# Performance work log

Hardware: AMD Instinct MI355X
Metric: run time of the kernel (lower is better)

Reference implementation:

```python
import jax, jax.numpy as jnp
import numpy as np

B, NCAP, LV, LT, C = 64, 64, 197, 32, 512
NSP = LV - 1          # 196 spatial patches
NUM_KEEP = 98         # ceil(196 * sparse_ratio=0.5)
KEEPED = 49           # int(196 * aggr_ratio=0.5 * sparse_ratio=0.5)
HID = 102             # int(512 * dim_ratio=0.2)
LN_EPS = 1e-5


def _normalize(x):
    # torch F.normalize: x / max(||x||, 1e-12)
    return x / jnp.maximum(jnp.linalg.norm(x, axis=-1, keepdims=True), 1e-12)


def setup_inputs() -> dict:
    key = jax.random.key(0)
    ks = jax.random.split(key, 8)
    def rn(k, shape, s=0.02):
        return jax.random.normal(k, shape, jnp.float32) * s
    return {
        "img_embs": jax.random.normal(ks[0], (B, LV, C), jnp.float32),
        "cap_embs": jax.random.normal(ks[1], (NCAP, LT, C), jnp.float32),
        "cap_lens": jnp.full((NCAP,), LT, jnp.int32),
        "ln_gamma": jnp.ones((C,), jnp.float32),
        "ln_beta": jnp.zeros((C,), jnp.float32),
        "w1": rn(ks[2], (C, HID)), "b1": jnp.zeros((HID,), jnp.float32),
        "w2": rn(ks[3], (HID, KEEPED)), "b2": jnp.zeros((KEEPED,), jnp.float32),
        "aggr_scale": jnp.ones((1, 1, 1), jnp.float32),
        "wi2t": rn(ks[4], (C, C)), "bi2t": jnp.zeros((C,), jnp.float32),
        "wt2i": rn(ks[5], (C, C)), "bt2i": jnp.zeros((C,), jnp.float32),
        "temp": jnp.ones((1, 1, 1), jnp.float32),
    }


def _forward(img_embs, cap_embs, ln_gamma, ln_beta, w1, b1, w2, b2,
             aggr_scale, wi2t, bi2t, wt2i, bt2i, temp):
    img_norm = _normalize(img_embs)
    img_cls = img_embs[:, 0:1]              # [B,1,C]  has_cls_token branch
    img_sp = img_embs[:, 1:]                # [B,196,C]
    img_sp_norm = img_norm[:, 1:]
    # use_cls_as_glob_embd: global = normalized CLS (no grad)
    glo = jax.lax.stop_gradient(img_norm[:, 0:1])
    attn_x = jax.lax.stop_gradient(jnp.sum(glo * img_sp_norm, -1))  # [B,196]
    cap_norm = _normalize(cap_embs)
    bidx = jnp.arange(B)[:, None]

    def ln(x):
        m = x.mean(-1, keepdims=True)
        v = jnp.var(x, axis=-1, keepdims=True)
        return (x - m) / jnp.sqrt(v + LN_EPS) * ln_gamma + ln_beta

    def per_caption(cap_i, cap_i_norm):
        # cap_i, cap_i_norm: [LT, C]
        cap_glo = jax.lax.stop_gradient(_normalize(cap_i[0:1]))           # [1,C]
        attn_y = jax.lax.stop_gradient(jnp.sum(cap_glo[None] * img_sp_norm, -1))  # [B,196]
        # --- TokenSparse ---
        score = attn_x + attn_y
        order = jnp.argsort(-score, axis=1)                              # descending
        keep, nonkeep = order[:, :NUM_KEEP], order[:, NUM_KEEP:]
        sel = img_sp[bidx, keep]                                          # [B,98,C]
        non = img_sp[bidx, nonkeep]                                       # [B,98,C]
        non_score = jnp.take_along_axis(score, nonkeep, 1)
        extra = jnp.sum(non * jax.nn.softmax(non_score, axis=1)[..., None],
                        axis=1, keepdims=True)                            # [B,1,C]
        # --- TokenAggregation ---
        h = jax.nn.gelu(ln(sel) @ w1 + b1, approximate=False)             # [B,98,HID]
        w = jnp.swapaxes(h @ w2 + b2, 1, 2) * aggr_scale                  # [B,49,98]
        aggr = jax.nn.softmax(w, axis=2) @ sel                            # [B,49,C]
        # [cls, aggr, extra] -> [B,51,C], then normalize
        sel_tok = _normalize(jnp.concatenate([img_cls, aggr, extra], 1))
        Ls = sel_tok.shape[1]
        # --- 'attn' similarity ---
        cap_exp = jnp.broadcast_to(cap_i_norm[None], (B, LT, C))
        st = jnp.swapaxes(sel_tok, 1, 2)                                  # [B,C,51]
        c2i = jax.nn.leaky_relu(cap_exp @ st, negative_slope=0.1)         # [B,LT,51]
        a_i2t = jax.nn.softmax((cap_exp @ wi2t + bi2t) @ st / temp, axis=1)
        a_t2i = jax.nn.softmax((cap_exp @ wt2i + bt2i) @ st / temp, axis=2)
        return jnp.sum(a_i2t * c2i / Ls + a_t2i * c2i / LT, axis=(1, 2))  # [B]

    sims = jax.vmap(per_caption)(cap_embs, cap_norm)                      # [NCAP,B]
    return sims.T                                                         # [B,NCAP]


def reference(img_embs, cap_embs, cap_lens, ln_gamma, ln_beta, w1, b1, w2, b2,
              aggr_scale, wi2t, bi2t, wt2i, bt2i, temp):
    # cap_lens are all LT (static shapes); eval-mode output: similarity matrix.
    return _forward(img_embs, cap_embs, ln_gamma, ln_beta, w1, b1, w2, b2,
                    aggr_scale, wi2t, bi2t, wt2i, bt2i, temp)
```

## Files before the change

### kernel.cpp

```cpp
#include <hip/hip_runtime.h>
#include <math.h>

#define B     64
#define NCAP  64
#define LV    197
#define LT    32
#define C     512
#define NSP   196
#define NKEEP 98
#define HID   102
#define KEEPED 49

#define OFF_ATTNX   12608
#define OFF_WSMAT   25152
#define OFF_WT      639808
#define OFF_GLOT    1688384
#define OFF_ATTNYT  1721152
#define OFF_IMGT    14164800
#define OFF_QBB     17834816
#define OFF_QCAP    19407680
#define OFF_W1TF    19931968
#define OFF_W2TF    19960640

typedef unsigned int u32;
typedef unsigned short u16;
typedef __bf16 bf16x8 __attribute__((ext_vector_type(8)));
typedef float f32x4 __attribute__((ext_vector_type(4)));
typedef unsigned int uint4v __attribute__((ext_vector_type(4)));

__device__ __forceinline__ u16 f2bf(float f) {
    u32 u = __builtin_bit_cast(u32, f);
    return (u16)((u + 0x7FFFu + ((u >> 16) & 1u)) >> 16);
}
__device__ __forceinline__ bf16x8 ld_bf8(const u16* p) {
    uint4v v = *reinterpret_cast<const uint4v*>(p);
    return __builtin_bit_cast(bf16x8, v);
}

__device__ __forceinline__ float gelu_exact(float x) {
    return 0.5f * x * (1.f + erff(x * 0.70710678118654752f));
}

__global__ __launch_bounds__(256) void k_pre(const float* __restrict__ cap,
                                             const float* __restrict__ wi2t,
                                             const float* __restrict__ wt2i,
                                             const float* __restrict__ w1,
                                             const float* __restrict__ w2,
                                             float* __restrict__ gloT,
                                             u16* __restrict__ Qbbf,
                                             u16* __restrict__ Qcap,
                                             u16* __restrict__ wT,
                                             u16* __restrict__ w1Tf,
                                             u16* __restrict__ w2Tf) {
    int idx = blockIdx.x, t = threadIdx.x;
    __shared__ __align__(16) u16 shb[64 * 65];

    if (idx < 512) {
        int e = idx, i = e >> 3, tg = e & 7;
        int lane = t & 63, wv = t >> 6;
        int tt = tg * 4 + wv;
        const float* row = cap + ((size_t)i * LT + tt) * C;
        float v[8]; float ss = 0.f;
#pragma unroll
        for (int q = 0; q < 8; ++q) { v[q] = row[lane + 64 * q]; ss += v[q] * v[q]; }
        for (int o = 32; o > 0; o >>= 1) ss += __shfl_down(ss, o);
        ss = __shfl(ss, 0);
        float inv = 1.f / fmaxf(sqrtf(ss), 1e-12f);
        u16* qrow = Qcap + ((size_t)i * 32 + tt) * C;
        int mi = tt >> 4, l15f = tt & 15;
        u16* qfb = Qbbf + (size_t)(i * 6 + mi) * 16 * 512;
#pragma unroll
        for (int q = 0; q < 8; ++q) {
            float n = v[q] * inv;
            u16 nb = f2bf(n);
            int c = lane + 64 * q;
            qrow[c] = nb;
            int ks = c >> 5, quadf = (c >> 3) & 3, jf = c & 7;
            qfb[(size_t)ks * 512 + (quadf * 16 + l15f) * 8 + jf] = nb;
            if (tt == 0) gloT[(c >> 2) * (NCAP * 4) + i * 4 + (c & 3)] = n;
        }
    } else if (idx < 640) {
        int e = idx - 512;
        int mat = e >> 6, ty = e & 63, jg = ty >> 3, cg = ty & 7;
        const float* W = mat ? wt2i : wi2t;
        u16 (*tile)[65] = (u16(*)[65])shb;
        for (int f = t; f < 4096; f += 256) {
            int cc2 = f >> 6, jj = f & 63;
            tile[jj][cc2] = f2bf(W[(size_t)(cg * 64 + cc2) * 512 + jg * 64 + jj]);
        }
        __syncthreads();
        for (int f = t; f < 4096; f += 256) {
            int jj = f >> 6, cc2 = f & 63;
            wT[((size_t)mat * 512 + jg * 64 + jj) * 512 + cg * 64 + cc2] = tile[jj][cc2];
        }
    } else if (idx < 647) {
        int nt = idx - 640;
        u32* outp = (u32*)w1Tf + (size_t)nt * 16 * 256;
        for (int f = t; f < 16 * 256; f += 256) {
            int ks = f >> 8, g = f & 255;
            int lane_o = g >> 2, j2 = g & 3;
            int l15o = lane_o & 15, quado = lane_o >> 4;
            int kk = ks * 32 + quado * 8 + 2 * j2;
            int n = nt * 16 + l15o;
            u32 lo = 0, hi = 0;
            if (n < HID) {
                lo = f2bf(w1[(size_t)kk * HID + n]);
                hi = f2bf(w1[(size_t)(kk + 1) * HID + n]);
            }
            outp[ks * 256 + g] = lo | (hi << 16);
        }
    } else {
        u32* outp = (u32*)w2Tf;
        for (int f = t; f < 16 * 256; f += 256) {
            int tile = f >> 8, g = f & 255;
            int nt2 = tile >> 2, ks2 = tile & 3;
            int lane_o = g >> 2, j2 = g & 3;
            int l15o = lane_o & 15, quado = lane_o >> 4;
            int kk0 = ks2 * 32 + quado * 8 + 2 * j2;
            int n = nt2 * 16 + l15o;
            u32 lo = 0, hi = 0;
            if (n < KEEPED) {
                if (kk0 < HID)     lo = f2bf(w2[(size_t)kk0 * KEEPED + n]);
                if (kk0 + 1 < HID) hi = f2bf(w2[(size_t)(kk0 + 1) * KEEPED + n]);
            }
            outp[tile * 256 + g] = lo | (hi << 16);
        }
    }
}

__global__ __launch_bounds__(512) void k_mid(const float* __restrict__ img,
                                             const u16* __restrict__ wT,
                                             const float* __restrict__ bi2t,
                                             const float* __restrict__ bt2i,
                                             const u16* __restrict__ Qcap,
                                             u16* __restrict__ Qbbf,
                                             const u16* __restrict__ w1Tf,
                                             const u16* __restrict__ w2Tf,
                                             const float* __restrict__ gamw,
                                             const float* __restrict__ betw,
                                             const float* __restrict__ b1,
                                             const float* __restrict__ b2,
                                             const float* __restrict__ scale_p,
                                             const float* __restrict__ gloT,
                                             float* __restrict__ attn_x,
                                             u16* __restrict__ WsM16,
                                             float* __restrict__ attn_yT,
                                             u16* __restrict__ imgTf) {
    int idx = blockIdx.x, t = threadIdx.x;
    __shared__ __align__(16) u16 shu[64 * 224];

    if (idx < 256) {
        int i = idx & 63, p = idx >> 6;
        int lane = t & 63, wu = t >> 6;
        int l15 = lane & 15, quad = lane >> 4;
        int mat = wu >> 2;
        int miq = (wu >> 1) & 1;
        int nh  = wu & 1;
        int ni0 = p * 8 + nh * 4;
        const u16* Arow = Qcap + ((size_t)i * 32 + miq * 16 + l15) * 512;
        const u16* Wm   = wT + (size_t)mat * 512 * 512;
        f32x4 acc[4];
#pragma unroll
        for (int n = 0; n < 4; ++n) acc[n] = (f32x4){0.f, 0.f, 0.f, 0.f};
        bf16x8 A = ld_bf8(Arow + quad * 8);
        bf16x8 Bf[4];
#pragma unroll
        for (int n = 0; n < 4; ++n)
            Bf[n] = ld_bf8(Wm + (size_t)((ni0 + n) * 16 + l15) * 512 + quad * 8);
        for (int ks = 0; ks < 16; ++ks) {
            bf16x8 An; bf16x8 Bn[4];
            if (ks < 15) {
                An = ld_bf8(Arow + (ks + 1) * 32 + quad * 8);
#pragma unroll
                for (int n = 0; n < 4; ++n)
                    Bn[n] = ld_bf8(Wm + (size_t)((ni0 + n) * 16 + l15) * 512 + (ks + 1) * 32 + quad * 8);
            }
#pragma unroll
            for (int n = 0; n < 4; ++n)
                acc[n] = __builtin_amdgcn_mfma_f32_16x16x32_bf16(A, Bf[n], acc[n], 0, 0, 0);
            A = An;
#pragma unroll
            for (int n = 0; n < 4; ++n) Bf[n] = Bn[n];
        }
        const float* bias = mat ? bt2i : bi2t;
#pragma unroll
        for (int n = 0; n < 4; ++n) {
            int j = (ni0 + n) * 16 + l15;
            float bj = bias[j];
            int ksf = j >> 5, quadf = (j >> 3) & 3, jf = j & 7;
#pragma unroll
            for (int r = 0; r < 4; ++r) {
                int q = 32 + mat * 32 + miq * 16 + quad * 4 + r;
                int mi = q >> 4, l15f = q & 15;
                Qbbf[(size_t)((i * 6 + mi) * 16 + ksf) * 512 + (quadf * 16 + l15f) * 8 + jf]
                    = f2bf(acc[n][r] + bj);
            }
        }
    } else if (idx < 1088) {
        int e = idx - 256;
        int b = e / 13, sg = e - b * 13;
        int s0 = sg * 16;
        u16* LNb = shu;
        u16* Hb  = shu + 16 * 520;
        int lane = t & 63, wu = t >> 6;
        int l15 = lane & 15, quad = lane >> 4;

        {
            int rr0 = 2 * wu, rr1 = 2 * wu + 1;
            int sA = s0 + rr0, sB = s0 + rr1;
            int sAc = sA < NSP ? sA : NSP - 1;
            int sBc = sB < NSP ? sB : NSP - 1;
            const float* rowA = img + ((size_t)b * LV + 1 + sAc) * C;
            const float* rowB = img + ((size_t)b * LV + 1 + sBc) * C;
            const float* cls  = img + (size_t)b * LV * C;
            float v0[8], v1[8];
            float sm0 = 0, ss0 = 0, dd0 = 0, sm1 = 0, ss1 = 0, dd1 = 0, sc = 0;
#pragma unroll
            for (int q = 0; q < 8; ++q) {
                int c = lane + 64 * q;
                float cv = cls[c];
                v0[q] = rowA[c]; v1[q] = rowB[c];
                sm0 += v0[q]; ss0 += v0[q] * v0[q]; dd0 += v0[q] * cv;
                sm1 += v1[q]; ss1 += v1[q] * v1[q]; dd1 += v1[q] * cv;
                sc  += cv * cv;
            }
            for (int o = 32; o > 0; o >>= 1) {
                sm0 += __shfl_down(sm0, o); ss0 += __shfl_down(ss0, o); dd0 += __shfl_down(dd0, o);
                sm1 += __shfl_down(sm1, o); ss1 += __shfl_down(ss1, o); dd1 += __shfl_down(dd1, o);
                sc  += __shfl_down(sc, o);
            }
            sm0 = __shfl(sm0, 0); ss0 = __shfl(ss0, 0);
            sm1 = __shfl(sm1, 0); ss1 = __shfl(ss1, 0);
            float mean0 = sm0 * (1.f / C);
            float rstd0 = 1.f / sqrtf(ss0 * (1.f / C) - mean0 * mean0 + 1e-5f);
            float mean1 = sm1 * (1.f / C);
            float rstd1 = 1.f / sqrtf(ss1 * (1.f / C) - mean1 * mean1 + 1e-5f);
            if (lane == 0) {
                float inv0 = 1.f / fmaxf(sqrtf(sc), 1e-12f);
                if (sA < NSP) attn_x[b * NSP + sA] = dd0 * inv0 * (1.f / fmaxf(sqrtf(ss0), 1e-12f));
                if (sB < NSP) attn_x[b * NSP + sB] = dd1 * inv0 * (1.f / fmaxf(sqrtf(ss1), 1e-12f));
            }
#pragma unroll
            for (int q = 0; q < 8; ++q) {
                int c = lane + 64 * q;
                float g = gamw[c], be = betw[c];
                LNb[rr0 * 520 + c] = f2bf((v0[q] - mean0) * rstd0 * g + be);
                LNb[rr1 * 520 + c] = f2bf((v1[q] - mean1) * rstd1 * g + be);
            }
        }
        __syncthreads();
        if (wu < 7) {
            const u16* W1b = w1Tf + (size_t)wu * 16 * 512;
            f32x4 h4 = (f32x4){0.f, 0.f, 0.f, 0.f};
            for (int ks = 0; ks < 16; ++ks) {
                bf16x8 A = ld_bf8(LNb + l15 * 520 + ks * 32 + quad * 8);
                bf16x8 Bv = ld_bf8(W1b + ks * 512 + lane * 8);
                h4 = __builtin_amdgcn_mfma_f32_16x16x32_bf16(A, Bv, h4, 0, 0, 0);
            }
            int col = wu * 16 + l15;
            if (col < HID) {
                float bb = b1[col];
#pragma unroll
                for (int r = 0; r < 4; ++r)
                    Hb[(quad * 4 + r) * 136 + col] = f2bf(gelu_exact(h4[r] + bb));
            } else {
#pragma unroll
                for (int r = 0; r < 4; ++r) Hb[(quad * 4 + r) * 136 + col] = 0;
            }
        } else {
            for (int f = lane; f < 16 * 24; f += 64) {
                int row = f / 24, cc = 112 + f % 24;
                Hb[row * 136 + cc] = 0;
            }
        }
        __syncthreads();
        if (wu < 4) {
            const u16* W2b = w2Tf + (size_t)wu * 4 * 512;
            f32x4 a2 = (f32x4){0.f, 0.f, 0.f, 0.f};
            for (int ks2 = 0; ks2 < 4; ++ks2) {
                bf16x8 A2 = ld_bf8(Hb + l15 * 136 + ks2 * 32 + quad * 8);
                bf16x8 B2 = ld_bf8(W2b + ks2 * 512 + lane * 8);
                a2 = __builtin_amdgcn_mfma_f32_16x16x32_bf16(A2, B2, a2, 0, 0, 0);
            }
            int k = wu * 16 + l15;
            if (k < KEEPED) {
                float scale = scale_p[0], bk = b2[k];
#pragma unroll
                for (int r = 0; r < 4; ++r) {
                    int row = quad * 4 + r;
                    if (s0 + row < NSP)
                        WsM16[((size_t)b * NSP + s0 + row) * 49 + k] = f2bf(expf((a2[r] + bk) * scale));
                }
            }
        }
    } else if (idx < 2688) {
        int e = idx - 1088;
        int b = e / 25;
        int s0 = (e - b * 25) * 8;
        int R = NSP - s0; if (R > 8) R = 8;
        float (*xr)[C] = (float(*)[C])shu;
        float* rnorm = (float*)shu + 4096;

        for (int f = t; f < R * C; f += 512) {
            int rr = f >> 9, c = f & 511;
            xr[rr][c] = img[((size_t)b * LV + 1 + s0 + rr) * C + c];
        }
        __syncthreads();
        {
            int row = t >> 6, l = t & 63;
            if (row < R) {
                float ss = 0.f;
                for (int c = l; c < C; c += 64) { float v = xr[row][c]; ss += v * v; }
                for (int o = 32; o > 0; o >>= 1) ss += __shfl_down(ss, o);
                if (l == 0) rnorm[row] = 1.f / fmaxf(sqrtf(ss), 1e-12f);
            }
        }
        __syncthreads();
        for (int f = t; f < R * C; f += 512) {
            int rr = f >> 9, c = f & 511;
            xr[rr][c] *= rnorm[rr];
        }
        __syncthreads();
        int i = t & 63, w = t >> 6;
        if (w < R) {
            float a0 = 0.f;
            const float4* g4 = (const float4*)gloT;
            const float4* x4 = (const float4*)xr[w];
            for (int c4 = 0; c4 < C / 4; ++c4) {
                float4 g = g4[c4 * NCAP + i];
                float4 x0 = x4[c4];
                a0 += x0.x * g.x + x0.y * g.y + x0.z * g.z + x0.w * g.w;
            }
            attn_yT[((size_t)b * NCAP + i) * NSP + s0 + w] = a0;
        }
    } else {
        int e = idx - 2688;
        int b = e >> 3, cg = e & 7;
        for (int f = t; f < 64 * 27; f += 512) shu[(f / 27) * 224 + 197 + (f % 27)] = 0;
        int cc = t & 63;
        for (int sb = t >> 6; sb < 197; sb += 8) {
            float v = img[((size_t)b * LV + sb) * C + cg * 64 + cc];
            shu[cc * 224 + sb] = f2bf(v);
        }
        __syncthreads();
        const u32* Tu = (const u32*)shu;
        u32* outp = (u32*)imgTf + (size_t)b * 7 * 32 * 256;
        for (int f = t; f < 7 * 4 * 256; f += 512) {
            int ks = f >> 10, rem = f & 1023;
            int ctl = rem >> 8, g = rem & 255;
            int lane_o = g >> 2, j2 = g & 3;
            int quad_o = lane_o >> 4, l15_o = lane_o & 15;
            int ccl = ctl * 16 + l15_o;
            int s = ks * 32 + quad_o * 8 + 2 * j2;
            u32 v = Tu[ccl * 112 + (s >> 1)];
            outp[(size_t)(ks * 32 + cg * 4 + ctl) * 256 + g] = v;
        }
    }
}

__global__ __launch_bounds__(512, 4) void k_main(const float* __restrict__ attn_x,
                                                 const float* __restrict__ attn_yT,
                                                 const u16* __restrict__ WsM16,
                                                 const u16* __restrict__ imgTf,
                                                 const u16* __restrict__ Qbbf,
                                                 const float* __restrict__ temp_p,
                                                 float* __restrict__ out) {
    int lin = blockIdx.x + NCAP * blockIdx.y;
    int b = (lin & 7) * 8 + ((lin >> 3) & 7);
    int i = lin >> 6;
    int t = threadIdx.x;
    int lane = t & 63, wu = t >> 6;
    int l15 = lane & 15, quad = lane >> 4;

    __shared__ __align__(16) u16 TnBuf[51 * 520];
    __shared__ float invn[64];
    __shared__ float redw[8];

    u16*   Pf   = TnBuf;
    float* ULDS = (float*)TnBuf;
    float* scoreS = (float*)(TnBuf + 24000);
    short* rnkH   = (short*)(TnBuf + 24392);
    u16*   keepL  = (u16*)  (TnBuf + 24784);
    u16*   nonL   = (u16*)  (TnBuf + 24882);
    float* snon   = (float*)(TnBuf + 25000);
    float* rowsq  = (float*)(TnBuf + 25372);

    const u16* imgTb = imgTf + (size_t)b * 7 * 32 * 512;
    bf16x8 Bc[4], Bn[4];
#pragma unroll
    for (int nj = 0; nj < 4; ++nj)
        Bc[nj] = ld_bf8(imgTb + (size_t)(wu * 4 + nj) * 512 + lane * 8);

    {
        uint4v* Pfv = (uint4v*)Pf;
        for (int f = t; f < 51 * 232 / 8; f += 512) Pfv[f] = (uint4v){0, 0, 0, 0};
    }
    if (t < NSP)
        scoreS[t] = attn_x[b * NSP + t] + attn_yT[((size_t)b * NCAP + i) * NSP + t];
    __syncthreads();
    if (t < 2 * NSP) {
        int half = (t >= NSP) ? 1 : 0;
        int s = t - half * NSP;
        float sv = scoreS[s];
        const float2* sc2 = (const float2*)scoreS;
        int base = half ? 49 : 0;
        int r = 0;
        for (int u2 = base; u2 < base + 49; ++u2) {
            float2 o = sc2[u2];
            int u = 2 * u2;
            r += (o.x > sv) || (o.x == sv && u < s);
            r += (o.y > sv) || (o.y == sv && (u + 1) < s);
        }
        rnkH[half * NSP + s] = (short)r;
    }
    __syncthreads();
    if (t < NSP) {
        int r = rnkH[t] + rnkH[NSP + t];
        if (r < NKEEP) keepL[r] = (u16)t;
        else { nonL[r - NKEEP] = (u16)t; snon[r - NKEEP] = scoreS[t]; }
    }
    __syncthreads();
    if (t == 0) Pf[0] = 0x3F80;
    if (t < NKEEP) Pf[50 * 232 + 1 + nonL[t]] = f2bf(expf(snon[t]));
    {
        int j = t / KEEPED, k = t - (t / KEEPED) * KEEPED;
#pragma unroll
        for (int it = 0; it < 10; ++it) {
            if (j < NKEEP) {
                int s = keepL[j];
                Pf[(1 + k) * 232 + 1 + s] = WsM16[((size_t)b * NSP + s) * 49 + k];
            }
            j += 10; k += 22;
            if (k >= KEEPED) { k -= KEEPED; ++j; }
        }
    }
    __syncthreads();

    f32x4 acc[4][4];
#pragma unroll
    for (int mi = 0; mi < 4; ++mi)
#pragma unroll
        for (int nj = 0; nj < 4; ++nj) acc[mi][nj] = (f32x4){0.f, 0.f, 0.f, 0.f};

    for (int ks = 0; ks < 7; ++ks) {
        if (ks < 6) {
#pragma unroll
            for (int nj = 0; nj < 4; ++nj)
                Bn[nj] = ld_bf8(imgTb + (size_t)((ks + 1) * 32 + wu * 4 + nj) * 512 + lane * 8);
        }
        bf16x8 Afr[4];
#pragma unroll
        for (int mi = 0; mi < 4; ++mi)
            Afr[mi] = ld_bf8(Pf + (mi * 16 + l15) * 232 + ks * 32 + quad * 8);
#pragma unroll
        for (int nj = 0; nj < 4; ++nj)
#pragma unroll
            for (int mi = 0; mi < 4; ++mi)
                acc[mi][nj] = __builtin_amdgcn_mfma_f32_16x16x32_bf16(Afr[mi], Bc[nj], acc[mi][nj], 0, 0, 0);
#pragma unroll
        for (int nj = 0; nj < 4; ++nj) Bc[nj] = Bn[nj];
    }

#pragma unroll
    for (int mi = 0; mi < 4; ++mi)
#pragma unroll
        for (int r = 0; r < 4; ++r) {
            float s = acc[mi][0][r] * acc[mi][0][r] + acc[mi][1][r] * acc[mi][1][r]
                    + acc[mi][2][r] * acc[mi][2][r] + acc[mi][3][r] * acc[mi][3][r];
            s += __shfl_down(s, 8); s += __shfl_down(s, 4);
            s += __shfl_down(s, 2); s += __shfl_down(s, 1);
            if (l15 == 0) rowsq[wu * 64 + mi * 16 + quad * 4 + r] = s;
        }
    __syncthreads();
    if (t < 64) {
        float s = 0.f;
#pragma unroll
        for (int w2 = 0; w2 < 8; ++w2) s += rowsq[w2 * 64 + t];
        invn[t] = 1.f / fmaxf(sqrtf(s), 1e-12f);
    }
    __syncthreads();

#pragma unroll
    for (int mi = 0; mi < 4; ++mi)
#pragma unroll
        for (int r = 0; r < 4; ++r) {
            int row = mi * 16 + quad * 4 + r;
            if (row < 51) {
                float iv = invn[row];
#pragma unroll
                for (int nj = 0; nj < 4; ++nj)
                    TnBuf[row * 520 + (wu * 4 + nj) * 16 + l15] = f2bf(acc[mi][nj][r] * iv);
            }
        }
    __syncthreads();

    const u16* Qbf = Qbbf + (size_t)i * 6 * 16 * 512;
    f32x4 ua[3];
#pragma unroll
    for (int e = 0; e < 3; ++e) ua[e] = (f32x4){0.f, 0.f, 0.f, 0.f};

    if (wu < 6) {
        const u16* Ar = Qbf + (size_t)wu * 16 * 512 + lane * 8;
        bf16x8 Aa = ld_bf8(Ar + 0 * 512);
        bf16x8 Ab = ld_bf8(Ar + 1 * 512);
        bf16x8 Ac = ld_bf8(Ar + 2 * 512);
        bf16x8 Ad = ld_bf8(Ar + 3 * 512);
#pragma unroll
        for (int g = 0; g < 4; ++g) {
            bf16x8 Na, Nb, Nc, Nd;
            if (g < 3) {
                Na = ld_bf8(Ar + (g * 4 + 4) * 512);
                Nb = ld_bf8(Ar + (g * 4 + 5) * 512);
                Nc = ld_bf8(Ar + (g * 4 + 6) * 512);
                Nd = ld_bf8(Ar + (g * 4 + 7) * 512);
            }
#pragma unroll
            for (int e = 0; e < 3; ++e) {
                const u16* Tb = TnBuf + (e * 16 + l15) * 520 + quad * 8;
                ua[e] = __builtin_amdgcn_mfma_f32_16x16x32_bf16(Aa, ld_bf8(Tb + (g * 4 + 0) * 32), ua[e], 0, 0, 0);
                ua[e] = __builtin_amdgcn_mfma_f32_16x16x32_bf16(Ab, ld_bf8(Tb + (g * 4 + 1) * 32), ua[e], 0, 0, 0);
                ua[e] = __builtin_amdgcn_mfma_f32_16x16x32_bf16(Ac, ld_bf8(Tb + (g * 4 + 2) * 32), ua[e], 0, 0, 0);
                ua[e] = __builtin_amdgcn_mfma_f32_16x16x32_bf16(Ad, ld_bf8(Tb + (g * 4 + 3) * 32), ua[e], 0, 0, 0);
            }
            Aa = Na; Ab = Nb; Ac = Nc; Ad = Nd;
        }
    } else {
        int w2 = wu - 6;
        int rowB = 48 + l15; if (rowB > 50) rowB = 50;
        const u16* Ar0 = Qbf + (size_t)(3 * w2 + 0) * 16 * 512 + lane * 8;
        const u16* Ar1 = Qbf + (size_t)(3 * w2 + 1) * 16 * 512 + lane * 8;
        const u16* Ar2 = Qbf + (size_t)(3 * w2 + 2) * 16 * 512 + lane * 8;
        bf16x8 Af0 = ld_bf8(Ar0);
        bf16x8 Af1 = ld_bf8(Ar1);
        bf16x8 Af2 = ld_bf8(Ar2);
        for (int ks = 0; ks < 16; ++ks) {
            bf16x8 An0, An1, An2;
            if (ks < 15) {
                An0 = ld_bf8(Ar0 + (ks + 1) * 512);
                An1 = ld_bf8(Ar1 + (ks + 1) * 512);
                An2 = ld_bf8(Ar2 + (ks + 1) * 512);
            }
            bf16x8 Bf = ld_bf8(TnBuf + rowB * 520 + ks * 32 + quad * 8);
            ua[0] = __builtin_amdgcn_mfma_f32_16x16x32_bf16(Af0, Bf, ua[0], 0, 0, 0);
            ua[1] = __builtin_amdgcn_mfma_f32_16x16x32_bf16(Af1, Bf, ua[1], 0, 0, 0);
            ua[2] = __builtin_amdgcn_mfma_f32_16x16x32_bf16(Af2, Bf, ua[2], 0, 0, 0);
            Af0 = An0; Af1 = An1; Af2 = An2;
        }
    }
    __syncthreads();

    if (wu < 6) {
#pragma unroll
        for (int e = 0; e < 3; ++e) {
            int l = e * 16 + l15;
            int q0 = wu * 16 + quad * 4;
#pragma unroll
            for (int r = 0; r < 4; ++r) ULDS[(q0 + r) * 52 + l] = ua[e][r];
        }
    } else {
        int l = 48 + l15;
        if (l < 51) {
            int w2 = wu - 6;
#pragma unroll
            for (int e = 0; e < 3; ++e) {
                int q0 = (3 * w2 + e) * 16 + quad * 4;
#pragma unroll
                for (int r = 0; r < 4; ++r) ULDS[(q0 + r) * 52 + l] = ua[e][r];
            }
        }
    }
    __syncthreads();

    float invT = 1.f / temp_p[0];
    if (t < 408) {
        int l = t >> 3, sub = t & 7;
        float vbuf[4]; float mm = -1e30f;
#pragma unroll
        for (int q = 0; q < 4; ++q) {
            float v = ULDS[(32 + sub + 8 * q) * 52 + l] * invT;
            vbuf[q] = v;
            mm = fmaxf(mm, v);
        }
#pragma unroll
        for (int o = 1; o < 8; o <<= 1) mm = fmaxf(mm, __shfl_xor(mm, o, 8));
        float e[4]; float z = 0.f;
#pragma unroll
        for (int q = 0; q < 4; ++q) { e[q] = expf(vbuf[q] - mm); z += e[q]; }
#pragma unroll
        for (int o = 1; o < 8; o <<= 1) z += __shfl_xor(z, o, 8);
        float iz = 1.f / z;
#pragma unroll
        for (int q = 0; q < 4; ++q) ULDS[(32 + sub + 8 * q) * 52 + l] = e[q] * iz;
    }
    if (t < 256) {
        int u = t >> 3, sub = t & 7;
        float vbuf[7]; int cnt = 0; float mm = -1e30f;
        for (int l = sub; l < 51; l += 8) {
            float v = ULDS[(64 + u) * 52 + l] * invT;
            vbuf[cnt++] = v;
            mm = fmaxf(mm, v);
        }
#pragma unroll
        for (int o = 1; o < 8; o <<= 1) mm = fmaxf(mm, __shfl_xor(mm, o, 8));
        float e[7]; float z = 0.f;
        for (int q = 0; q < cnt; ++q) { e[q] = expf(vbuf[q] - mm); z += e[q]; }
#pragma unroll
        for (int o = 1; o < 8; o <<= 1) z += __shfl_xor(z, o, 8);
        float iz = 1.f / z;
        { int q = 0;
          for (int l = sub; l < 51; l += 8) { ULDS[(64 + u) * 52 + l] = e[q] * iz; ++q; } }
    }
    __syncthreads();

    float part = 0.f;
    {
        int u = t / 51, l = t - (t / 51) * 51;
        while (u < LT) {
            float u0 = ULDS[u * 52 + l];
            float c2 = (u0 > 0.f) ? u0 : 0.1f * u0;
            float av = ULDS[(32 + u) * 52 + l];
            float bv = ULDS[(64 + u) * 52 + l];
            part += c2 * (av * (1.f / 51.f) + bv * (1.f / 32.f));
            u += 10; l += 2;
            if (l >= 51) { l -= 51; ++u; }
        }
    }
    for (int o = 32; o > 0; o >>= 1) part += __shfl_down(part, o);
    if (lane == 0) redw[wu] = part;
    __syncthreads();
    if (t == 0) {
        float s = 0.f;
#pragma unroll
        for (int w2 = 0; w2 < 8; ++w2) s += redw[w2];
        out[b * NCAP + i] = s;
    }
}

extern "C" void kernel_launch(void* const* d_in, const int* in_sizes, int n_in,
                              void* d_out, int out_size, void* d_ws, size_t ws_size,
                              hipStream_t stream) {
    const float* img        = (const float*)d_in[0];
    const float* cap        = (const float*)d_in[1];
    const float* gamw       = (const float*)d_in[3];
    const float* betw       = (const float*)d_in[4];
    const float* w1         = (const float*)d_in[5];
    const float* b1         = (const float*)d_in[6];
    const float* w2         = (const float*)d_in[7];
    const float* b2         = (const float*)d_in[8];
    const float* aggr_scale = (const float*)d_in[9];
    const float* wi2t       = (const float*)d_in[10];
    const float* bi2t       = (const float*)d_in[11];
    const float* wt2i       = (const float*)d_in[12];
    const float* bt2i       = (const float*)d_in[13];
    const float* temp       = (const float*)d_in[14];
    float* out = (float*)d_out;

    float* ws      = (float*)d_ws;
    float* attn_x  = ws + OFF_ATTNX;
    u16*   WsM16   = (u16*)(ws + OFF_WSMAT);
    u16*   wT      = (u16*)(ws + OFF_WT);
    float* gloT    = ws + OFF_GLOT;
    float* attn_yT = ws + OFF_ATTNYT;
    u16*   imgTf   = (u16*)(ws + OFF_IMGT);
    u16*   Qbbf    = (u16*)(ws + OFF_QBB);
    u16*   Qcap    = (u16*)(ws + OFF_QCAP);
    u16*   w1Tf    = (u16*)(ws + OFF_W1TF);
    u16*   w2Tf    = (u16*)(ws + OFF_W2TF);

    k_pre<<<dim3(648), dim3(256), 0, stream>>>(cap, wi2t, wt2i, w1, w2,
                                               gloT, Qbbf, Qcap, wT, w1Tf, w2Tf);
    k_mid<<<dim3(3200), dim3(512), 0, stream>>>(img, wT, bi2t, bt2i, Qcap, Qbbf,
                                                w1Tf, w2Tf, gamw, betw, b1, b2, aggr_scale,
                                                gloT, attn_x, WsM16, attn_yT, imgTf);
    k_main<<<dim3(NCAP, B), dim3(512), 0, stream>>>(attn_x, attn_yT, WsM16, imgTf, Qbbf, temp, out);
}
```

Baseline: 344.0 us.

## Split token GEMM into two row halves to cut registers and raise occupancy

Launch bounds move from 4 to 6 blocks per SM. To fit that register budget, the 64-row token aggregation GEMM is split into two passes of 32 rows each (upper rows first, then lower), halving the accumulator array, and the row-norm scratch is reused in LDS. Register prefetch double-buffering is dropped in both GEMM phases. The imgT B-fragments are now loaded from global twice, and the lost software pipelining may expose latency, in exchange for more resident waves.

```diff
diff --git a/kernel.cpp b/kernel.cpp
--- a/kernel.cpp
+++ b/kernel.cpp
@@ -358,7 +358,7 @@
     }
 }
 
-__global__ __launch_bounds__(512, 4) void k_main(const float* __restrict__ attn_x,
+__global__ __launch_bounds__(512, 6) void k_main(const float* __restrict__ attn_x,
                                                  const float* __restrict__ attn_yT,
                                                  const u16* __restrict__ WsM16,
                                                  const u16* __restrict__ imgTf,
@@ -383,13 +383,10 @@
     u16*   keepL  = (u16*)  (TnBuf + 24784);
     u16*   nonL   = (u16*)  (TnBuf + 24882);
     float* snon   = (float*)(TnBuf + 25000);
-    float* rowsq  = (float*)(TnBuf + 25372);
+    float* rowsqA = (float*)(TnBuf + 25372);
+    float* rowsqB = (float*)TnBuf;
 
     const u16* imgTb = imgTf + (size_t)b * 7 * 32 * 512;
-    bf16x8 Bc[4], Bn[4];
-#pragma unroll
-    for (int nj = 0; nj < 4; ++nj)
-        Bc[nj] = ld_bf8(imgTb + (size_t)(wu * 4 + nj) * 512 + lane * 8);
 
     {
         uint4v* Pfv = (uint4v*)Pf;
@@ -436,61 +433,102 @@
     }
     __syncthreads();
 
-    f32x4 acc[4][4];
-#pragma unroll
-    for (int mi = 0; mi < 4; ++mi)
-#pragma unroll
-        for (int nj = 0; nj < 4; ++nj) acc[mi][nj] = (f32x4){0.f, 0.f, 0.f, 0.f};
+    f32x4 acc2[2][4];
+#pragma unroll
+    for (int m = 0; m < 2; ++m)
+#pragma unroll
+        for (int nj = 0; nj < 4; ++nj) acc2[m][nj] = (f32x4){0.f, 0.f, 0.f, 0.f};
 
     for (int ks = 0; ks < 7; ++ks) {
-        if (ks < 6) {
-#pragma unroll
-            for (int nj = 0; nj < 4; ++nj)
-                Bn[nj] = ld_bf8(imgTb + (size_t)((ks + 1) * 32 + wu * 4 + nj) * 512 + lane * 8);
-        }
-        bf16x8 Afr[4];
-#pragma unroll
-        for (int mi = 0; mi < 4; ++mi)
-            Afr[mi] = ld_bf8(Pf + (mi * 16 + l15) * 232 + ks * 32 + quad * 8);
+        bf16x8 Bc[4];
 #pragma unroll
         for (int nj = 0; nj < 4; ++nj)
-#pragma unroll
-            for (int mi = 0; mi < 4; ++mi)
-                acc[mi][nj] = __builtin_amdgcn_mfma_f32_16x16x32_bf16(Afr[mi], Bc[nj], acc[mi][nj], 0, 0, 0);
-#pragma unroll
-        for (int nj = 0; nj < 4; ++nj) Bc[nj] = Bn[nj];
-    }
-
-#pragma unroll
-    for (int mi = 0; mi < 4; ++mi)
+            Bc[nj] = ld_bf8(imgTb + (size_t)(ks * 32 + wu * 4 + nj) * 512 + lane * 8);
+        bf16x8 Af0 = ld_bf8(Pf + (32 + l15) * 232 + ks * 32 + quad * 8);
+        bf16x8 Af1 = ld_bf8(Pf + (48 + l15) * 232 + ks * 32 + quad * 8);
+#pragma unroll
+        for (int nj = 0; nj < 4; ++nj) {
+            acc2[0][nj] = __builtin_amdgcn_mfma_f32_16x16x32_bf16(Af0, Bc[nj], acc2[0][nj], 0, 0, 0);
+            acc2[1][nj] = __builtin_amdgcn_mfma_f32_16x16x32_bf16(Af1, Bc[nj], acc2[1][nj], 0, 0, 0);
+        }
+    }
+#pragma unroll
+    for (int m = 0; m < 2; ++m)
 #pragma unroll
         for (int r = 0; r < 4; ++r) {
-            float s = acc[mi][0][r] * acc[mi][0][r] + acc[mi][1][r] * acc[mi][1][r]
-                    + acc[mi][2][r] * acc[mi][2][r] + acc[mi][3][r] * acc[mi][3][r];
+            float s = acc2[m][0][r] * acc2[m][0][r] + acc2[m][1][r] * acc2[m][1][r]
+                    + acc2[m][2][r] * acc2[m][2][r] + acc2[m][3][r] * acc2[m][3][r];
             s += __shfl_down(s, 8); s += __shfl_down(s, 4);
             s += __shfl_down(s, 2); s += __shfl_down(s, 1);
-            if (l15 == 0) rowsq[wu * 64 + mi * 16 + quad * 4 + r] = s;
-        }
-    __syncthreads();
-    if (t < 64) {
+            if (l15 == 0) rowsqA[wu * 32 + m * 16 + quad * 4 + r] = s;
+        }
+    __syncthreads();
+    if (t < 32) {
         float s = 0.f;
 #pragma unroll
-        for (int w2 = 0; w2 < 8; ++w2) s += rowsq[w2 * 64 + t];
-        invn[t] = 1.f / fmaxf(sqrtf(s), 1e-12f);
-    }
-    __syncthreads();
-
-#pragma unroll
-    for (int mi = 0; mi < 4; ++mi)
+        for (int w2 = 0; w2 < 8; ++w2) s += rowsqA[w2 * 32 + t];
+        invn[32 + t] = 1.f / fmaxf(sqrtf(s), 1e-12f);
+    }
+    __syncthreads();
+#pragma unroll
+    for (int m = 0; m < 2; ++m)
 #pragma unroll
         for (int r = 0; r < 4; ++r) {
-            int row = mi * 16 + quad * 4 + r;
+            int row = 32 + m * 16 + quad * 4 + r;
             if (row < 51) {
                 float iv = invn[row];
 #pragma unroll
                 for (int nj = 0; nj < 4; ++nj)
-                    TnBuf[row * 520 + (wu * 4 + nj) * 16 + l15] = f2bf(acc[mi][nj][r] * iv);
-            }
+                    TnBuf[row * 520 + (wu * 4 + nj) * 16 + l15] = f2bf(acc2[m][nj][r] * iv);
+            }
+        }
+
+#pragma unroll
+    for (int m = 0; m < 2; ++m)
+#pragma unroll
+        for (int nj = 0; nj < 4; ++nj) acc2[m][nj] = (f32x4){0.f, 0.f, 0.f, 0.f};
+
+    for (int ks = 0; ks < 7; ++ks) {
+        bf16x8 Bc[4];
+#pragma unroll
+        for (int nj = 0; nj < 4; ++nj)
+            Bc[nj] = ld_bf8(imgTb + (size_t)(ks * 32 + wu * 4 + nj) * 512 + lane * 8);
+        bf16x8 Af0 = ld_bf8(Pf + (0 + l15) * 232 + ks * 32 + quad * 8);
+        bf16x8 Af1 = ld_bf8(Pf + (16 + l15) * 232 + ks * 32 + quad * 8);
+#pragma unroll
+        for (int nj = 0; nj < 4; ++nj) {
+            acc2[0][nj] = __builtin_amdgcn_mfma_f32_16x16x32_bf16(Af0, Bc[nj], acc2[0][nj], 0, 0, 0);
+            acc2[1][nj] = __builtin_amdgcn_mfma_f32_16x16x32_bf16(Af1, Bc[nj], acc2[1][nj], 0, 0, 0);
+        }
+    }
+    __syncthreads();
+#pragma unroll
+    for (int m = 0; m < 2; ++m)
+#pragma unroll
+        for (int r = 0; r < 4; ++r) {
+            float s = acc2[m][0][r] * acc2[m][0][r] + acc2[m][1][r] * acc2[m][1][r]
+                    + acc2[m][2][r] * acc2[m][2][r] + acc2[m][3][r] * acc2[m][3][r];
+            s += __shfl_down(s, 8); s += __shfl_down(s, 4);
+            s += __shfl_down(s, 2); s += __shfl_down(s, 1);
+            if (l15 == 0) rowsqB[wu * 32 + m * 16 + quad * 4 + r] = s;
+        }
+    __syncthreads();
+    if (t < 32) {
+        float s = 0.f;
+#pragma unroll
+        for (int w2 = 0; w2 < 8; ++w2) s += rowsqB[w2 * 32 + t];
+        invn[t] = 1.f / fmaxf(sqrtf(s), 1e-12f);
+    }
+    __syncthreads();
+#pragma unroll
+    for (int m = 0; m < 2; ++m)
+#pragma unroll
+        for (int r = 0; r < 4; ++r) {
+            int row = m * 16 + quad * 4 + r;
+            float iv = invn[row];
+#pragma unroll
+            for (int nj = 0; nj < 4; ++nj)
+                TnBuf[row * 520 + (wu * 4 + nj) * 16 + l15] = f2bf(acc2[m][nj][r] * iv);
         }
     __syncthreads();
 
@@ -501,28 +539,16 @@
 
     if (wu < 6) {
         const u16* Ar = Qbf + (size_t)wu * 16 * 512 + lane * 8;
-        bf16x8 Aa = ld_bf8(Ar + 0 * 512);
-        bf16x8 Ab = ld_bf8(Ar + 1 * 512);
-        bf16x8 Ac = ld_bf8(Ar + 2 * 512);
-        bf16x8 Ad = ld_bf8(Ar + 3 * 512);
-#pragma unroll
-        for (int g = 0; g < 4; ++g) {
-            bf16x8 Na, Nb, Nc, Nd;
-            if (g < 3) {
-                Na = ld_bf8(Ar + (g * 4 + 4) * 512);
-                Nb = ld_bf8(Ar + (g * 4 + 5) * 512);
-                Nc = ld_bf8(Ar + (g * 4 + 6) * 512);
-                Nd = ld_bf8(Ar + (g * 4 + 7) * 512);
-            }
+        bf16x8 Af = ld_bf8(Ar);
+        for (int ks = 0; ks < 16; ++ks) {
+            bf16x8 An;
+            if (ks < 15) An = ld_bf8(Ar + (ks + 1) * 512);
 #pragma unroll
             for (int e = 0; e < 3; ++e) {
-                const u16* Tb = TnBuf + (e * 16 + l15) * 520 + quad * 8;
-                ua[e] = __builtin_amdgcn_mfma_f32_16x16x32_bf16(Aa, ld_bf8(Tb + (g * 4 + 0) * 32), ua[e], 0, 0, 0);
-                ua[e] = __builtin_amdgcn_mfma_f32_16x16x32_bf16(Ab, ld_bf8(Tb + (g * 4 + 1) * 32), ua[e], 0, 0, 0);
-                ua[e] = __builtin_amdgcn_mfma_f32_16x16x32_bf16(Ac, ld_bf8(Tb + (g * 4 + 2) * 32), ua[e], 0, 0, 0);
-                ua[e] = __builtin_amdgcn_mfma_f32_16x16x32_bf16(Ad, ld_bf8(Tb + (g * 4 + 3) * 32), ua[e], 0, 0, 0);
-            }
-            Aa = Na; Ab = Nb; Ac = Nc; Ad = Nd;
+                bf16x8 Bf = ld_bf8(TnBuf + (e * 16 + l15) * 520 + ks * 32 + quad * 8);
+                ua[e] = __builtin_amdgcn_mfma_f32_16x16x32_bf16(Af, Bf, ua[e], 0, 0, 0);
+            }
+            Af = An;
         }
     } else {
         int w2 = wu - 6;
@@ -530,21 +556,11 @@
         const u16* Ar0 = Qbf + (size_t)(3 * w2 + 0) * 16 * 512 + lane * 8;
         const u16* Ar1 = Qbf + (size_t)(3 * w2 + 1) * 16 * 512 + lane * 8;
         const u16* Ar2 = Qbf + (size_t)(3 * w2 + 2) * 16 * 512 + lane * 8;
-        bf16x8 Af0 = ld_bf8(Ar0);
-        bf16x8 Af1 = ld_bf8(Ar1);
-        bf16x8 Af2 = ld_bf8(Ar2);
         for (int ks = 0; ks < 16; ++ks) {
-            bf16x8 An0, An1, An2;
-            if (ks < 15) {
-                An0 = ld_bf8(Ar0 + (ks + 1) * 512);
-                An1 = ld_bf8(Ar1 + (ks + 1) * 512);
-                An2 = ld_bf8(Ar2 + (ks + 1) * 512);
-            }
             bf16x8 Bf = ld_bf8(TnBuf + rowB * 520 + ks * 32 + quad * 8);
-            ua[0] = __builtin_amdgcn_mfma_f32_16x16x32_bf16(Af0, Bf, ua[0], 0, 0, 0);
-            ua[1] = __builtin_amdgcn_mfma_f32_16x16x32_bf16(Af1, Bf, ua[1], 0, 0, 0);
-            ua[2] = __builtin_amdgcn_mfma_f32_16x16x32_bf16(Af2, Bf, ua[2], 0, 0, 0);
-            Af0 = An0; Af1 = An1; Af2 = An2;
+            ua[0] = __builtin_amdgcn_mfma_f32_16x16x32_bf16(ld_bf8(Ar0 + ks * 512), Bf, ua[0], 0, 0, 0);
+            ua[1] = __builtin_amdgcn_mfma_f32_16x16x32_bf16(ld_bf8(Ar1 + ks * 512), Bf, ua[1], 0, 0, 0);
+            ua[2] = __builtin_amdgcn_mfma_f32_16x16x32_bf16(ld_bf8(Ar2 + ks * 512), Bf, ua[2], 0, 0, 0);
         }
     }
     __syncthreads();
```

Result: slower. 402.2 us (+16.9%).
